# Kernel tuning notes

Hardware: AMD Instinct MI355X
Metric: run time of the kernel (lower is better)

Reference implementation:

```python
import jax, jax.numpy as jnp
import numpy as np

LAYERS = [1024, 2048, 1024]
OPTIONS = 4
BATCH = 2048


def setup_inputs() -> dict:
    key = jax.random.key(0)
    k_x, k_idx, k_w1, k_w2 = jax.random.split(key, 4)
    x = jax.random.normal(k_x, (BATCH, LAYERS[0]), dtype=jnp.float32)
    idx = jax.random.randint(k_idx, (BATCH,), 0, OPTIONS, dtype=jnp.int64)
    # xavier-normal-ish scaled weights per layer: shape [options, in, out]
    std1 = float(np.sqrt(2.0 / (LAYERS[0] * LAYERS[1] + OPTIONS * LAYERS[1])))
    std2 = float(np.sqrt(2.0 / (LAYERS[1] * LAYERS[2] + OPTIONS * LAYERS[2])))
    W1 = jax.random.normal(k_w1, (OPTIONS, LAYERS[0], LAYERS[1]), dtype=jnp.float32) * std1
    b1 = jnp.zeros((OPTIONS, LAYERS[1]), dtype=jnp.float32)
    W2 = jax.random.normal(k_w2, (OPTIONS, LAYERS[1], LAYERS[2]), dtype=jnp.float32) * std2
    b2 = jnp.zeros((OPTIONS, LAYERS[2]), dtype=jnp.float32)
    return {"x": x, "idx": idx, "W1": W1, "b1": b1, "W2": W2, "b2": b2}


def reference(x, idx, W1, b1, W2, b2):
    # Original: torch.bmm(x[:,None,:], W[idx]) + b[zeros_like(idx)]
    # Equivalent math without materializing the [B, in, out] gathered weights:
    # compute all options densely, then select per-sample option with idx.
    # NOTE: bias is ALWAYS option 0 (faithful to the original's zeros_like(idx)).
    def layer(h, W, b):
        h_all = jnp.einsum('bi,oij->boj', h, W)  # [B, O, out]
        h_sel = jnp.take_along_axis(h_all, idx[:, None, None], axis=1)[:, 0, :]  # [B, out]
        return h_sel + b[0][None, :]

    h = layer(x, W1, b1)
    out = layer(h, W2, b2)
    return out
```

## Files before the change

### kernel.cpp

```cpp
#include <hip/hip_runtime.h>
#include <stdint.h>

typedef __bf16 bf16x8 __attribute__((ext_vector_type(8)));
typedef float f32x4 __attribute__((ext_vector_type(4)));
typedef unsigned short u16;
typedef const __attribute__((address_space(1))) void* as1_cvp;
typedef __attribute__((address_space(3))) void* as3_vp;

__device__ __forceinline__ u16 f2bf(float f) {
  union { float f; unsigned u; } v; v.f = f;
  unsigned r = v.u + 0x7fffu + ((v.u >> 16) & 1u);
  return (u16)(r >> 16);
}

__global__ __launch_bounds__(256) void hist_perm_kernel(
    const int* __restrict__ idx, int n, int* __restrict__ starts,
    int* __restrict__ perm, int* __restrict__ tmap128,
    int* __restrict__ tmap64) {
  __shared__ int cnt[4][256];
  __shared__ int gtot[4], gstart[4];
  const int t = threadIdx.x;
  const int rpt = (n + 255) >> 8;
  const int base = t * rpt;
  int c[4] = {0, 0, 0, 0};
  for (int j = 0; j < rpt; ++j) {
    const int i = base + j;
    if (i < n) c[idx[i] & 3]++;
  }
  #pragma unroll
  for (int g = 0; g < 4; ++g) cnt[g][t] = c[g];
  __syncthreads();
  const int w = t >> 6, l = t & 63;
  {
    const int s0 = cnt[w][l * 4 + 0], s1 = cnt[w][l * 4 + 1];
    const int s2 = cnt[w][l * 4 + 2], s3 = cnt[w][l * 4 + 3];
    const int sum = s0 + s1 + s2 + s3;
    int sc = sum;
    #pragma unroll
    for (int d = 1; d < 64; d <<= 1) {
      const int o = __shfl_up(sc, d, 64);
      if (l >= d) sc += o;
    }
    const int ex = sc - sum;
    cnt[w][l * 4 + 0] = ex;
    cnt[w][l * 4 + 1] = ex + s0;
    cnt[w][l * 4 + 2] = ex + s0 + s1;
    cnt[w][l * 4 + 3] = ex + s0 + s1 + s2;
    if (l == 63) gtot[w] = sc;
  }
  __syncthreads();
  if (t == 0) {
    int s = 0, nt128 = 0, nt64 = 0;
    for (int g = 0; g < 4; ++g) {
      gstart[g] = s;
      starts[g] = s;
      const int cg = gtot[g];
      for (int j = 0; j < cg; j += 128) tmap128[nt128++] = (g << 28) | (s + j);
      for (int j = 0; j < cg; j += 64)  tmap64[nt64++]  = (g << 28) | (s + j);
      s += cg;
    }
    starts[4] = s;
    while (nt128 < 20) tmap128[nt128++] = -1;
    while (nt64 < 40)  tmap64[nt64++]  = -1;
  }
  __syncthreads();
  int run[4] = {0, 0, 0, 0};
  for (int j = 0; j < rpt; ++j) {
    const int i = base + j;
    if (i < n) {
      const int g = idx[i] & 3;
      perm[gstart[g] + cnt[g][t] + run[g]] = i;
      run[g]++;
    }
  }
}

__device__ __forceinline__ void wtrans_body(
    float (*tile)[65], const float* __restrict__ W, u16* __restrict__ WT,
    int K, int N, int tx, int ty, int o) {
  const float* Wo = W + (size_t)o * K * N;
  u16* WTo = WT + (size_t)o * N * K;
  const int k0 = ty * 64, n0 = tx * 64;
  const int rr = threadIdx.x >> 4, cc = threadIdx.x & 15;
  #pragma unroll
  for (int j = 0; j < 4; ++j) {
    const int r = j * 16 + rr;
    const float4 v = *(const float4*)(Wo + (size_t)(k0 + r) * N + n0 + cc * 4);
    tile[r][cc * 4 + 0] = v.x; tile[r][cc * 4 + 1] = v.y;
    tile[r][cc * 4 + 2] = v.z; tile[r][cc * 4 + 3] = v.w;
  }
  __syncthreads();
  #pragma unroll
  for (int j = 0; j < 4; ++j) {
    const int nrow = j * 16 + rr;
    ushort4 u;
    u.x = f2bf(tile[cc * 4 + 0][nrow]);
    u.y = f2bf(tile[cc * 4 + 1][nrow]);
    u.z = f2bf(tile[cc * 4 + 2][nrow]);
    u.w = f2bf(tile[cc * 4 + 3][nrow]);
    *(ushort4*)(WTo + (size_t)(n0 + nrow) * K + k0 + cc * 4) = u;
  }
}

__global__ __launch_bounds__(256) void w1t_gather_kernel(
    const float* __restrict__ W1, u16* __restrict__ W1T,
    const float* __restrict__ x, const int* __restrict__ perm,
    u16* __restrict__ Xs) {
  __shared__ float tile[64][65];
  const int bid = blockIdx.x;
  if (bid >= 2048) {
    const int p = bid - 2048;
    const int b = perm[p];
    const float4 v = ((const float4*)(x + (size_t)b * 1024))[threadIdx.x];
    ushort4 u;
    u.x = f2bf(v.x); u.y = f2bf(v.y); u.z = f2bf(v.z); u.w = f2bf(v.w);
    ((ushort4*)(Xs + (size_t)p * 1024))[threadIdx.x] = u;
    return;
  }
  const int xcd = bid & 7, i = bid >> 3;
  const int tx = (xcd << 2) | (i & 3);
  const int ty = (i >> 2) & 15;
  const int o = i >> 6;
  wtrans_body(tile, W1, W1T, 1024, 2048, tx, ty, o);
}

template <int EPI, int TM, int NT_PAD, int KT, int NN, int NTN>
__device__ __forceinline__ void gemm_body(
    char* smem, int bid,
    const u16* __restrict__ A, const u16* __restrict__ BT,
    const float* __restrict__ bias, const int* __restrict__ starts,
    const int* __restrict__ tmap, const int* __restrict__ perm,
    u16* __restrict__ outH, float* __restrict__ outF) {
  constexpr int MR = TM / 32;
  constexpr int ABUF = TM * 128;
  constexpr int BSTR = ABUF + 16384;

  const int nwg = NT_PAD * NTN;
  const int q = nwg >> 3;
  const int swz = (bid & 7) * q + (bid >> 3);
  const int tile = swz % NT_PAD;
  const int n_t = swz / NT_PAD;

  const int tm = tmap[tile];
  if (tm < 0) return;
  const int o = tm >> 28;
  const int m_start = tm & 0x0FFFFFFF;
  const int g1 = starts[o + 1];
  const int n_start = n_t * 128;
  const u16* Bo = BT + (size_t)o * NN * KT;

  const int tid = threadIdx.x;
  const int w = tid >> 6;
  const int l = tid & 63;
  const int wm = w >> 1, wn = w & 1;
  const int l8 = l & 7, ld8 = l >> 3;

  const int src_unit = l8 ^ (ld8 & 7);

  const u16* pA[MR];
  #pragma unroll
  for (int j = 0; j < MR; ++j) {
    int r = m_start + (j * 4 + w) * 8 + ld8;
    if (r >= g1) r = g1 - 1;
    pA[j] = A + (size_t)r * KT + src_unit * 8;
  }
  const u16* pB[4];
  #pragma unroll
  for (int j = 0; j < 4; ++j) {
    const int nr = n_start + (j * 4 + w) * 8 + ld8;
    pB[j] = Bo + (size_t)nr * KT + src_unit * 8;
  }

#define STAGE(dst_off)                                                         \
  {                                                                            \
    _Pragma("unroll")                                                          \
    for (int j = 0; j < MR; ++j)                                               \
      __builtin_amdgcn_global_load_lds((as1_cvp)pA[j],                         \
          (as3_vp)(smem + (dst_off) + (j * 4 + w) * 1024), 16, 0, 0);          \
    _Pragma("unroll")                                                          \
    for (int j = 0; j < 4; ++j)                                                \
      __builtin_amdgcn_global_load_lds((as1_cvp)pB[j],                         \
          (as3_vp)(smem + (dst_off) + ABUF + (j * 4 + w) * 1024), 16, 0, 0);   \
    _Pragma("unroll") for (int j = 0; j < MR; ++j) pA[j] += 64;                \
    _Pragma("unroll") for (int j = 0; j < 4; ++j) pB[j] += 64;                 \
  }

  const int lrow = l & 15;
  const int lx = l & 7;
  const int lu = l >> 4;
  int offA[MR][2], offB[4][2];
  #pragma unroll
  for (int a = 0; a < MR; ++a)
    #pragma unroll
    for (int kk = 0; kk < 2; ++kk)
      offA[a][kk] = (wm * (TM / 2) + a * 16 + lrow) * 128 + (((kk * 4 + lu) ^ lx) << 4);
  #pragma unroll
  for (int b = 0; b < 4; ++b)
    #pragma unroll
    for (int kk = 0; kk < 2; ++kk)
      offB[b][kk] = (wn * 64 + b * 16 + lrow) * 128 + (((kk * 4 + lu) ^ lx) << 4);

  f32x4 acc[MR][4] = {};

  const int nK = KT >> 6;
  STAGE(0);
  for (int kt = 0; kt < nK; ++kt) {
    const int cur = (kt & 1) * BSTR;
    if (kt + 1 < nK) {
      STAGE(BSTR - cur);
      if constexpr (TM == 128)
        asm volatile("s_waitcnt vmcnt(8)" ::: "memory");
      else
        asm volatile("s_waitcnt vmcnt(6)" ::: "memory");
    } else {
      asm volatile("s_waitcnt vmcnt(0)" ::: "memory");
    }
    __builtin_amdgcn_s_barrier();

    bf16x8 af[MR][2], bfr[4][2];
    #pragma unroll
    for (int a = 0; a < MR; ++a)
      #pragma unroll
      for (int kk = 0; kk < 2; ++kk)
        af[a][kk] = *(const bf16x8*)(smem + cur + offA[a][kk]);
    #pragma unroll
    for (int b = 0; b < 4; ++b)
      #pragma unroll
      for (int kk = 0; kk < 2; ++kk)
        bfr[b][kk] = *(const bf16x8*)(smem + cur + ABUF + offB[b][kk]);
    asm volatile("s_waitcnt lgkmcnt(0)" ::: "memory");
    __builtin_amdgcn_s_barrier();

    __builtin_amdgcn_s_setprio(1);
    #pragma unroll
    for (int kk = 0; kk < 2; ++kk)
      #pragma unroll
      for (int a = 0; a < MR; ++a)
        #pragma unroll
        for (int b = 0; b < 4; ++b)
          acc[a][b] = __builtin_amdgcn_mfma_f32_16x16x32_bf16(af[a][kk], bfr[b][kk], acc[a][b], 0, 0, 0);
    __builtin_amdgcn_s_setprio(0);
  }
#undef STAGE

  const int col_l = l & 15;
  const int row_l = (l >> 4) << 2;
  #pragma unroll
  for (int a = 0; a < MR; ++a) {
    #pragma unroll
    for (int b = 0; b < 4; ++b) {
      const int n = n_start + wn * 64 + b * 16 + col_l;
      const float bv = bias[n];
      #pragma unroll
      for (int r = 0; r < 4; ++r) {
        const int p = m_start + wm * (TM / 2) + a * 16 + row_l + r;
        if (p < g1) {
          if (EPI == 0) {
            outH[(size_t)p * NN + n] = f2bf(acc[a][b][r] + bv);
          } else {
            outF[(size_t)perm[p] * NN + n] = acc[a][b][r] + bv;
          }
        }
      }
    }
  }
}

__global__ __launch_bounds__(256, 2) void gemm1_w2t_kernel(
    const u16* __restrict__ Xs, const u16* __restrict__ W1T,
    const float* __restrict__ b1, const int* __restrict__ starts,
    const int* __restrict__ tmap128, u16* __restrict__ Hs,
    const float* __restrict__ W2, u16* __restrict__ W2T) {
  __shared__ char smem[65536];
  const int bid = blockIdx.x;
  if (bid < 320) {
    gemm_body<0, 128, 20, 1024, 2048, 16>(
        smem, bid, Xs, W1T, b1, starts, tmap128, nullptr, Hs, nullptr);
  } else {
    const int b = bid - 320;
    const int xcd = b & 7, i = b >> 3;
    const int tx = (xcd << 1) | (i & 1);
    const int ty = (i >> 1) & 31;
    const int o = i >> 6;
    wtrans_body((float(*)[65])smem, W2, W2T, 2048, 1024, tx, ty, o);
  }
}

__global__ __launch_bounds__(256, 2) void gemm2_kernel(
    const u16* __restrict__ Hs, const u16* __restrict__ W2T,
    const float* __restrict__ b2, const int* __restrict__ starts,
    const int* __restrict__ tmap64, const int* __restrict__ perm,
    float* __restrict__ out) {
  __shared__ char smem[49152];
  gemm_body<1, 64, 40, 2048, 1024, 8>(
      smem, blockIdx.x, Hs, W2T, b2, starts, tmap64, perm, nullptr, out);
}

extern "C" void kernel_launch(void* const* d_in, const int* in_sizes, int n_in,
                              void* d_out, int out_size, void* d_ws, size_t ws_size,
                              hipStream_t stream) {
  (void)n_in; (void)out_size; (void)ws_size;
  const float* x   = (const float*)d_in[0];
  const int*   idx = (const int*)d_in[1];
  const float* W1  = (const float*)d_in[2];
  const float* b1  = (const float*)d_in[3];
  const float* W2  = (const float*)d_in[4];
  const float* b2  = (const float*)d_in[5];
  float* out = (float*)d_out;

  const int B = in_sizes[1];

  char* ws = (char*)d_ws;
  u16* W1T     = (u16*)(ws);
  u16* W2T     = (u16*)(ws + 16777216);
  u16* Xs      = (u16*)(ws + 33554432);
  u16* Hs      = (u16*)(ws + 37748736);
  int* perm    = (int*)(ws + 46137344);
  int* starts  = (int*)(ws + 46137344 + 8192);
  int* tmap128 = starts + 64;
  int* tmap64  = starts + 128;

  hist_perm_kernel<<<1, 256, 0, stream>>>(idx, B, starts, perm, tmap128, tmap64);
  w1t_gather_kernel<<<2048 + B, 256, 0, stream>>>(W1, W1T, x, perm, Xs);
  gemm1_w2t_kernel<<<320 + 2048, 256, 0, stream>>>(
      Xs, W1T, b1, starts, tmap128, Hs, W2, W2T);
  gemm2_kernel<<<320, 256, 0, stream>>>(Hs, W2T, b2, starts, tmap64, perm, out);
}
```

Baseline: 72.73 us.

## Rewrite GEMM1 mainloop as 4-stage K=32 pipeline with single barrier

Splits the templated GEMM into separate GEMM1 and GEMM2 bodies. GEMM1 now stages K-slices of 32 instead of 64 into a 4-deep ring of 16KB LDS buffers, keeping three slices in flight with graded vmcnt waits. It uses one barrier per iteration instead of two, and issues the next stage's loads after the fragment reads so they overlap the MFMAs. GEMM1 also gets a new swizzle layout for the 64-byte rows. The cost is more loop iterations with fewer MFMAs each, and correctness now depends on the ring depth protecting buffer reuse without the second barrier.

```diff
diff --git a/kernel.cpp b/kernel.cpp
--- a/kernel.cpp
+++ b/kernel.cpp
@@ -124,16 +124,13 @@
   wtrans_body(tile, W1, W1T, 1024, 2048, tx, ty, o);
 }
 
-template <int EPI, int TM, int NT_PAD, int KT, int NN, int NTN>
-__device__ __forceinline__ void gemm_body(
+__device__ __forceinline__ void gemm1_body(
     char* smem, int bid,
     const u16* __restrict__ A, const u16* __restrict__ BT,
     const float* __restrict__ bias, const int* __restrict__ starts,
-    const int* __restrict__ tmap, const int* __restrict__ perm,
-    u16* __restrict__ outH, float* __restrict__ outF) {
-  constexpr int MR = TM / 32;
-  constexpr int ABUF = TM * 128;
-  constexpr int BSTR = ABUF + 16384;
+    const int* __restrict__ tmap, u16* __restrict__ outH) {
+  constexpr int NT_PAD = 20, NTN = 16, KT = 1024, NN = 2048;
+  constexpr int BSTR = 16384;
 
   const int nwg = NT_PAD * NTN;
   const int q = nwg >> 3;
@@ -153,8 +150,124 @@
   const int w = tid >> 6;
   const int l = tid & 63;
   const int wm = w >> 1, wn = w & 1;
+
+  const int su = ((l & 3) ^ ((l >> 2) & 3)) << 3;
+  const u16* pA[2];
+  #pragma unroll
+  for (int j = 0; j < 2; ++j) {
+    int r = m_start + (w * 2 + j) * 16 + (l >> 2);
+    if (r >= g1) r = g1 - 1;
+    pA[j] = A + (size_t)r * KT + su;
+  }
+  const u16* pB[2];
+  #pragma unroll
+  for (int j = 0; j < 2; ++j) {
+    const int nr = n_start + (w * 2 + j) * 16 + (l >> 2);
+    pB[j] = Bo + (size_t)nr * KT + su;
+  }
+
+#define STAGE32(dst_off)                                                       \
+  {                                                                            \
+    _Pragma("unroll")                                                          \
+    for (int j = 0; j < 2; ++j)                                                \
+      __builtin_amdgcn_global_load_lds((as1_cvp)pA[j],                         \
+          (as3_vp)(smem + (dst_off) + (w * 2 + j) * 1024), 16, 0, 0);          \
+    _Pragma("unroll")                                                          \
+    for (int j = 0; j < 2; ++j)                                                \
+      __builtin_amdgcn_global_load_lds((as1_cvp)pB[j],                         \
+          (as3_vp)(smem + (dst_off) + 8192 + (w * 2 + j) * 1024), 16, 0, 0);   \
+    _Pragma("unroll") for (int j = 0; j < 2; ++j) pA[j] += 32;                 \
+    _Pragma("unroll") for (int j = 0; j < 2; ++j) pB[j] += 32;                 \
+  }
+
+  const int ru = ((l >> 4) ^ (l & 3)) << 4;
+  const int lrow = l & 15;
+  int offA[4], offB[4];
+  #pragma unroll
+  for (int a = 0; a < 4; ++a)
+    offA[a] = (wm * 64 + a * 16 + lrow) * 64 + ru;
+  #pragma unroll
+  for (int b = 0; b < 4; ++b)
+    offB[b] = (wn * 64 + b * 16 + lrow) * 64 + ru + 8192;
+
+  f32x4 acc[4][4] = {};
+
+  const int nK = KT >> 5;
+  STAGE32(0); STAGE32(BSTR); STAGE32(2 * BSTR);
+  for (int t = 0; t < nK; ++t) {
+    const int cur = (t & 3) * BSTR;
+    if (t + 2 < nK)      asm volatile("s_waitcnt vmcnt(8)" ::: "memory");
+    else if (t + 1 < nK) asm volatile("s_waitcnt vmcnt(4)" ::: "memory");
+    else                 asm volatile("s_waitcnt vmcnt(0)" ::: "memory");
+    __builtin_amdgcn_s_barrier();
+
+    bf16x8 af[4], bfr[4];
+    #pragma unroll
+    for (int a = 0; a < 4; ++a)
+      af[a] = *(const bf16x8*)(smem + cur + offA[a]);
+    #pragma unroll
+    for (int b = 0; b < 4; ++b)
+      bfr[b] = *(const bf16x8*)(smem + cur + offB[b]);
+    if (t + 3 < nK) STAGE32(((t + 3) & 3) * BSTR);
+    asm volatile("s_waitcnt lgkmcnt(0)" ::: "memory");
+
+    __builtin_amdgcn_s_setprio(1);
+    #pragma unroll
+    for (int a = 0; a < 4; ++a)
+      #pragma unroll
+      for (int b = 0; b < 4; ++b)
+        acc[a][b] = __builtin_amdgcn_mfma_f32_16x16x32_bf16(af[a], bfr[b], acc[a][b], 0, 0, 0);
+    __builtin_amdgcn_s_setprio(0);
+  }
+#undef STAGE32
+
+  const int col_l = l & 15;
+  const int row_l = (l >> 4) << 2;
+  #pragma unroll
+  for (int a = 0; a < 4; ++a) {
+    #pragma unroll
+    for (int b = 0; b < 4; ++b) {
+      const int n = n_start + wn * 64 + b * 16 + col_l;
+      const float bv = bias[n];
+      #pragma unroll
+      for (int r = 0; r < 4; ++r) {
+        const int p = m_start + wm * 64 + a * 16 + row_l + r;
+        if (p < g1) outH[(size_t)p * NN + n] = f2bf(acc[a][b][r] + bv);
+      }
+    }
+  }
+}
+
+__device__ __forceinline__ void gemm2_body(
+    char* smem, int bid,
+    const u16* __restrict__ A, const u16* __restrict__ BT,
+    const float* __restrict__ bias, const int* __restrict__ starts,
+    const int* __restrict__ tmap, const int* __restrict__ perm,
+    float* __restrict__ outF) {
+  constexpr int TM = 64, NT_PAD = 40, KT = 2048, NN = 1024, NTN = 8;
+  constexpr int MR = TM / 32;
+  constexpr int ABUF = TM * 128;
+  constexpr int BSTR = ABUF + 16384;
+
+  const int nwg = NT_PAD * NTN;
+  const int q = nwg >> 3;
+  const int swz = (bid & 7) * q + (bid >> 3);
+  const int tile = swz % NT_PAD;
+  const int n_t = swz / NT_PAD;
+
+  const int tm = tmap[tile];
+  if (tm < 0) return;
+  const int o = tm >> 28;
+  const int m_start = tm & 0x0FFFFFFF;
+  const int g1 = starts[o + 1];
+  const int n_start = n_t * 128;
+  const u16* Bo = BT + (size_t)o * NN * KT;
+
+  const int tid = threadIdx.x;
+  const int w = tid >> 6;
+  const int l = tid & 63;
+  const int wm = w >> 1, wn = w & 1;
   const int l8 = l & 7, ld8 = l >> 3;
-
   const int src_unit = l8 ^ (ld8 & 7);
 
   const u16* pA[MR];
@@ -208,10 +321,7 @@
     const int cur = (kt & 1) * BSTR;
     if (kt + 1 < nK) {
       STAGE(BSTR - cur);
-      if constexpr (TM == 128)
-        asm volatile("s_waitcnt vmcnt(8)" ::: "memory");
-      else
-        asm volatile("s_waitcnt vmcnt(6)" ::: "memory");
+      asm volatile("s_waitcnt vmcnt(6)" ::: "memory");
     } else {
       asm volatile("s_waitcnt vmcnt(0)" ::: "memory");
     }
@@ -254,13 +364,7 @@
       #pragma unroll
       for (int r = 0; r < 4; ++r) {
         const int p = m_start + wm * (TM / 2) + a * 16 + row_l + r;
-        if (p < g1) {
-          if (EPI == 0) {
-            outH[(size_t)p * NN + n] = f2bf(acc[a][b][r] + bv);
-          } else {
-            outF[(size_t)perm[p] * NN + n] = acc[a][b][r] + bv;
-          }
-        }
+        if (p < g1) outF[(size_t)perm[p] * NN + n] = acc[a][b][r] + bv;
       }
     }
   }
@@ -274,8 +378,7 @@
   __shared__ char smem[65536];
   const int bid = blockIdx.x;
   if (bid < 320) {
-    gemm_body<0, 128, 20, 1024, 2048, 16>(
-        smem, bid, Xs, W1T, b1, starts, tmap128, nullptr, Hs, nullptr);
+    gemm1_body(smem, bid, Xs, W1T, b1, starts, tmap128, Hs);
   } else {
     const int b = bid - 320;
     const int xcd = b & 7, i = b >> 3;
@@ -292,8 +395,7 @@
     const int* __restrict__ tmap64, const int* __restrict__ perm,
     float* __restrict__ out) {
   __shared__ char smem[49152];
-  gemm_body<1, 64, 40, 2048, 1024, 8>(
-      smem, blockIdx.x, Hs, W2T, b2, starts, tmap64, perm, nullptr, out);
+  gemm2_body(smem, blockIdx.x, Hs, W2T, b2, starts, tmap64, perm, out);
 }
 
 extern "C" void kernel_launch(void* const* d_in, const int* in_sizes, int n_in,
```

Result: slower. 74.86 us (+2.9%).

## Split-K the second GEMM and fold histogram into W1 transpose launch

Applied to the files above, without the earlier changes.

The second grouped GEMM is split into two K halves, giving 640 workgroups instead of 320. Partial fp32 sums go to a scratch buffer that reuses the W1T region, and a new reduce kernel adds the halves and the bias, then scatters rows back through the permutation. Separately, the single-block histogram/permutation kernel is merged into the W1 transpose launch as an extra block, and the x gather becomes its own kernel. This trades one fewer serial launch and more GEMM2 parallelism against an extra kernel plus about 16MB of partial-sum traffic.

```diff
diff --git a/kernel.cpp b/kernel.cpp
--- a/kernel.cpp
+++ b/kernel.cpp
@@ -13,12 +13,13 @@
   return (u16)(r >> 16);
 }
 
-__global__ __launch_bounds__(256) void hist_perm_kernel(
-    const int* __restrict__ idx, int n, int* __restrict__ starts,
-    int* __restrict__ perm, int* __restrict__ tmap128,
-    int* __restrict__ tmap64) {
-  __shared__ int cnt[4][256];
-  __shared__ int gtot[4], gstart[4];
+__device__ void hist_body(const int* __restrict__ idx, int n,
+                          int* __restrict__ starts, int* __restrict__ perm,
+                          int* __restrict__ tmap128, int* __restrict__ tmap64,
+                          int* cnt , int* gmeta ) {
+  int (*c4)[256] = (int(*)[256])cnt;
+  int* gtot = gmeta;
+  int* gstart = gmeta + 4;
   const int t = threadIdx.x;
   const int rpt = (n + 255) >> 8;
   const int base = t * rpt;
@@ -28,12 +29,12 @@
     if (i < n) c[idx[i] & 3]++;
   }
   #pragma unroll
-  for (int g = 0; g < 4; ++g) cnt[g][t] = c[g];
+  for (int g = 0; g < 4; ++g) c4[g][t] = c[g];
   __syncthreads();
   const int w = t >> 6, l = t & 63;
   {
-    const int s0 = cnt[w][l * 4 + 0], s1 = cnt[w][l * 4 + 1];
-    const int s2 = cnt[w][l * 4 + 2], s3 = cnt[w][l * 4 + 3];
+    const int s0 = c4[w][l * 4 + 0], s1 = c4[w][l * 4 + 1];
+    const int s2 = c4[w][l * 4 + 2], s3 = c4[w][l * 4 + 3];
     const int sum = s0 + s1 + s2 + s3;
     int sc = sum;
     #pragma unroll
@@ -42,10 +43,10 @@
       if (l >= d) sc += o;
     }
     const int ex = sc - sum;
-    cnt[w][l * 4 + 0] = ex;
-    cnt[w][l * 4 + 1] = ex + s0;
-    cnt[w][l * 4 + 2] = ex + s0 + s1;
-    cnt[w][l * 4 + 3] = ex + s0 + s1 + s2;
+    c4[w][l * 4 + 0] = ex;
+    c4[w][l * 4 + 1] = ex + s0;
+    c4[w][l * 4 + 2] = ex + s0 + s1;
+    c4[w][l * 4 + 3] = ex + s0 + s1 + s2;
     if (l == 63) gtot[w] = sc;
   }
   __syncthreads();
@@ -69,7 +70,7 @@
     const int i = base + j;
     if (i < n) {
       const int g = idx[i] & 3;
-      perm[gstart[g] + cnt[g][t] + run[g]] = i;
+      perm[gstart[g] + c4[g][t] + run[g]] = i;
       run[g]++;
     }
   }
@@ -102,19 +103,16 @@
   }
 }
 
-__global__ __launch_bounds__(256) void w1t_gather_kernel(
+__global__ __launch_bounds__(256) void w1t_hist_kernel(
     const float* __restrict__ W1, u16* __restrict__ W1T,
-    const float* __restrict__ x, const int* __restrict__ perm,
-    u16* __restrict__ Xs) {
+    const int* __restrict__ idx, int n, int* __restrict__ starts,
+    int* __restrict__ perm, int* __restrict__ tmap128,
+    int* __restrict__ tmap64) {
   __shared__ float tile[64][65];
   const int bid = blockIdx.x;
-  if (bid >= 2048) {
-    const int p = bid - 2048;
-    const int b = perm[p];
-    const float4 v = ((const float4*)(x + (size_t)b * 1024))[threadIdx.x];
-    ushort4 u;
-    u.x = f2bf(v.x); u.y = f2bf(v.y); u.z = f2bf(v.z); u.w = f2bf(v.w);
-    ((ushort4*)(Xs + (size_t)p * 1024))[threadIdx.x] = u;
+  if (bid == 2048) {
+    hist_body(idx, n, starts, perm, tmap128, tmap64,
+              (int*)&tile[0][0], (int*)&tile[32][0]);
     return;
   }
   const int xcd = bid & 7, i = bid >> 3;
@@ -124,22 +122,35 @@
   wtrans_body(tile, W1, W1T, 1024, 2048, tx, ty, o);
 }
 
-template <int EPI, int TM, int NT_PAD, int KT, int NN, int NTN>
+__global__ __launch_bounds__(256) void gather_kernel(
+    const float* __restrict__ x, const int* __restrict__ perm,
+    u16* __restrict__ Xs) {
+  const int p = blockIdx.x;
+  const int b = perm[p];
+  const float4 v = ((const float4*)(x + (size_t)b * 1024))[threadIdx.x];
+  ushort4 u;
+  u.x = f2bf(v.x); u.y = f2bf(v.y); u.z = f2bf(v.z); u.w = f2bf(v.w);
+  ((ushort4*)(Xs + (size_t)p * 1024))[threadIdx.x] = u;
+}
+
+template <int EPI, int TM, int NT_PAD, int KT, int NN, int NTN, int SPLIT>
 __device__ __forceinline__ void gemm_body(
     char* smem, int bid,
     const u16* __restrict__ A, const u16* __restrict__ BT,
     const float* __restrict__ bias, const int* __restrict__ starts,
-    const int* __restrict__ tmap, const int* __restrict__ perm,
-    u16* __restrict__ outH, float* __restrict__ outF) {
+    const int* __restrict__ tmap, float* __restrict__ outP,
+    u16* __restrict__ outH) {
   constexpr int MR = TM / 32;
   constexpr int ABUF = TM * 128;
   constexpr int BSTR = ABUF + 16384;
 
-  const int nwg = NT_PAD * NTN;
+  const int nwg = NT_PAD * NTN * SPLIT;
   const int q = nwg >> 3;
   const int swz = (bid & 7) * q + (bid >> 3);
   const int tile = swz % NT_PAD;
-  const int n_t = swz / NT_PAD;
+  const int rest = swz / NT_PAD;
+  const int n_t = rest % NTN;
+  const int s = rest / NTN;
 
   const int tm = tmap[tile];
   if (tm < 0) return;
@@ -147,6 +158,7 @@
   const int m_start = tm & 0x0FFFFFFF;
   const int g1 = starts[o + 1];
   const int n_start = n_t * 128;
+  const int kb0 = s * (KT / SPLIT);
   const u16* Bo = BT + (size_t)o * NN * KT;
 
   const int tid = threadIdx.x;
@@ -162,13 +174,13 @@
   for (int j = 0; j < MR; ++j) {
     int r = m_start + (j * 4 + w) * 8 + ld8;
     if (r >= g1) r = g1 - 1;
-    pA[j] = A + (size_t)r * KT + src_unit * 8;
+    pA[j] = A + (size_t)r * KT + kb0 + src_unit * 8;
   }
   const u16* pB[4];
   #pragma unroll
   for (int j = 0; j < 4; ++j) {
     const int nr = n_start + (j * 4 + w) * 8 + ld8;
-    pB[j] = Bo + (size_t)nr * KT + src_unit * 8;
+    pB[j] = Bo + (size_t)nr * KT + kb0 + src_unit * 8;
   }
 
 #define STAGE(dst_off)                                                         \
@@ -202,7 +214,7 @@
 
   f32x4 acc[MR][4] = {};
 
-  const int nK = KT >> 6;
+  const int nK = (KT / SPLIT) >> 6;
   STAGE(0);
   for (int kt = 0; kt < nK; ++kt) {
     const int cur = (kt & 1) * BSTR;
@@ -250,7 +262,8 @@
     #pragma unroll
     for (int b = 0; b < 4; ++b) {
       const int n = n_start + wn * 64 + b * 16 + col_l;
-      const float bv = bias[n];
+      float bv = 0.f;
+      if (EPI == 0) bv = bias[n];
       #pragma unroll
       for (int r = 0; r < 4; ++r) {
         const int p = m_start + wm * (TM / 2) + a * 16 + row_l + r;
@@ -258,7 +271,7 @@
           if (EPI == 0) {
             outH[(size_t)p * NN + n] = f2bf(acc[a][b][r] + bv);
           } else {
-            outF[(size_t)perm[p] * NN + n] = acc[a][b][r] + bv;
+            outP[((size_t)(s * 2048 + p)) * NN + n] = acc[a][b][r];
           }
         }
       }
@@ -274,8 +287,8 @@
   __shared__ char smem[65536];
   const int bid = blockIdx.x;
   if (bid < 320) {
-    gemm_body<0, 128, 20, 1024, 2048, 16>(
-        smem, bid, Xs, W1T, b1, starts, tmap128, nullptr, Hs, nullptr);
+    gemm_body<0, 128, 20, 1024, 2048, 16, 1>(
+        smem, bid, Xs, W1T, b1, starts, tmap128, nullptr, Hs);
   } else {
     const int b = bid - 320;
     const int xcd = b & 7, i = b >> 3;
@@ -286,14 +299,29 @@
   }
 }
 
-__global__ __launch_bounds__(256, 2) void gemm2_kernel(
+__global__ __launch_bounds__(256, 2) void gemm2s_kernel(
     const u16* __restrict__ Hs, const u16* __restrict__ W2T,
-    const float* __restrict__ b2, const int* __restrict__ starts,
-    const int* __restrict__ tmap64, const int* __restrict__ perm,
-    float* __restrict__ out) {
+    const int* __restrict__ starts, const int* __restrict__ tmap64,
+    float* __restrict__ part) {
   __shared__ char smem[49152];
-  gemm_body<1, 64, 40, 2048, 1024, 8>(
-      smem, blockIdx.x, Hs, W2T, b2, starts, tmap64, perm, nullptr, out);
+  gemm_body<1, 64, 40, 2048, 1024, 8, 2>(
+      smem, blockIdx.x, Hs, W2T, nullptr, starts, tmap64, part, nullptr);
+}
+
+__global__ __launch_bounds__(256) void reduce_kernel(
+    const float* __restrict__ part, const float* __restrict__ b2,
+    const int* __restrict__ perm, float* __restrict__ out) {
+  const int p = blockIdx.x;
+  const int t = threadIdx.x;
+  const float4 v0 = ((const float4*)(part + (size_t)p * 1024))[t];
+  const float4 v1 = ((const float4*)(part + (size_t)(2048 + p) * 1024))[t];
+  const float4 bv = ((const float4*)b2)[t];
+  float4 r;
+  r.x = v0.x + v1.x + bv.x;
+  r.y = v0.y + v1.y + bv.y;
+  r.z = v0.z + v1.z + bv.z;
+  r.w = v0.w + v1.w + bv.w;
+  ((float4*)(out + (size_t)perm[p] * 1024))[t] = r;
 }
 
 extern "C" void kernel_launch(void* const* d_in, const int* in_sizes, int n_in,
@@ -312,6 +340,7 @@
 
   char* ws = (char*)d_ws;
   u16* W1T     = (u16*)(ws);
+  float* part  = (float*)(ws);
   u16* W2T     = (u16*)(ws + 16777216);
   u16* Xs      = (u16*)(ws + 33554432);
   u16* Hs      = (u16*)(ws + 37748736);
@@ -320,9 +349,11 @@
   int* tmap128 = starts + 64;
   int* tmap64  = starts + 128;
 
-  hist_perm_kernel<<<1, 256, 0, stream>>>(idx, B, starts, perm, tmap128, tmap64);
-  w1t_gather_kernel<<<2048 + B, 256, 0, stream>>>(W1, W1T, x, perm, Xs);
+  w1t_hist_kernel<<<2049, 256, 0, stream>>>(W1, W1T, idx, B, starts, perm,
+                                            tmap128, tmap64);
+  gather_kernel<<<B, 256, 0, stream>>>(x, perm, Xs);
   gemm1_w2t_kernel<<<320 + 2048, 256, 0, stream>>>(
       Xs, W1T, b1, starts, tmap128, Hs, W2, W2T);
-  gemm2_kernel<<<320, 256, 0, stream>>>(Hs, W2T, b2, starts, tmap64, perm, out);
-}
+  gemm2s_kernel<<<640, 256, 0, stream>>>(Hs, W2T, starts, tmap64, part);
+  reduce_kernel<<<B, 256, 0, stream>>>(part, b2, perm, out);
+}
```

Result: faster. 70.10 us (-3.6%).
